# Kernel tuning notes

Measured on AMD Instinct MI355X. Metric: run time of the kernel, lower is better.

Reference implementation:

```python
import jax, jax.numpy as jnp
import numpy as np


def setup_inputs() -> dict:
    key = jax.random.key(0)
    k1, k2 = jax.random.split(key)
    B, S, N, D = 4, 8, 2048, 3
    pred_points = jax.random.normal(k1, (B, S, N, D), dtype=jnp.float32)
    target_points = jax.random.normal(k2, (B, S, N, D), dtype=jnp.float32)
    return {"pred_points": pred_points, "target_points": target_points}


def reference(pred_points, target_points):
    # pred_points, target_points: [B, S, N, 3]
    seq_len = pred_points.shape[1]
    # Pairwise Euclidean distances via the GEMM identity |p-t|^2 = |p|^2 + |t|^2 - 2 p.t
    p2 = jnp.sum(pred_points * pred_points, axis=-1)      # [B,S,N]
    t2 = jnp.sum(target_points * target_points, axis=-1)  # [B,S,M]
    cross = jnp.einsum('bsnd,bsmd->bsnm', pred_points, target_points)  # [B,S,N,M]
    d2 = p2[..., :, None] + t2[..., None, :] - 2.0 * cross
    d = jnp.sqrt(jnp.maximum(d2, 0.0))  # [B,S,N,M]
    # Bidirectional nearest-neighbor min + mean over points
    min_p2t = jnp.min(d, axis=3)  # [B,S,N]
    min_t2p = jnp.min(d, axis=2)  # [B,S,M]
    chamfer = jnp.mean(min_p2t, axis=2) + jnp.mean(min_t2p, axis=2)  # [B,S]
    total_loss = jnp.sum(chamfer, axis=1)  # [B] (sum over timesteps)
    # reduction == 'mean'
    return jnp.mean(total_loss) / seq_len
```

## Files before the change

### kernel.cpp

```cpp
#include <hip/hip_runtime.h>
#include <math.h>

#define N_PTS   2048
#define BLOCK   256
#define NQ      8
#define SLAB    256
#define NSLAB   (N_PTS / SLAB)

__global__ __launch_bounds__(BLOCK) void chamfer_min_kernel(
    const float* __restrict__ pred,
    const float* __restrict__ tgt,
    unsigned int* __restrict__ wsmin)
{
    __shared__ float4 sh[SLAB];

    const int bs   = blockIdx.x;
    const int dir  = blockIdx.y;
    const int slab = blockIdx.z;
    const int tid  = threadIdx.x;

    const float* Abase = (dir ? tgt : pred) + (size_t)bs * N_PTS * 3;
    const float* Bbase = (dir ? pred : tgt) + (size_t)bs * N_PTS * 3;

    {
        const int j = slab * SLAB + tid;
        const float x = Bbase[3 * j + 0];
        const float y = Bbase[3 * j + 1];
        const float z = Bbase[3 * j + 2];
        sh[tid] = make_float4(x, y, z, x * x + y * y + z * z);
    }
    __syncthreads();

    float nx[NQ], ny[NQ], nz[NQ], p2[NQ], best[NQ];
    #pragma unroll
    for (int k = 0; k < NQ; ++k) {
        const int q = tid + BLOCK * k;
        const float px = Abase[3 * q + 0];
        const float py = Abase[3 * q + 1];
        const float pz = Abase[3 * q + 2];
        nx[k] = -2.0f * px;
        ny[k] = -2.0f * py;
        nz[k] = -2.0f * pz;
        p2[k] = px * px + py * py + pz * pz;
        best[k] = 3.4e38f;
    }

    #pragma unroll 2
    for (int j = 0; j < SLAB; j += 2) {
        const float4 t0 = sh[j];
        const float4 t1 = sh[j + 1];
        #pragma unroll
        for (int k = 0; k < NQ; ++k) {
            const float v0 = fmaf(nx[k], t0.x,
                             fmaf(ny[k], t0.y,
                             fmaf(nz[k], t0.z, t0.w)));
            const float v1 = fmaf(nx[k], t1.x,
                             fmaf(ny[k], t1.y,
                             fmaf(nz[k], t1.z, t1.w)));
            best[k] = fminf(fminf(best[k], v0), v1);
        }
    }

    const int base = (dir * 32 + bs) * N_PTS;
    #pragma unroll
    for (int k = 0; k < NQ; ++k) {
        const float d2 = fmaxf(p2[k] + best[k], 0.0f);
        atomicMin(&wsmin[base + tid + BLOCK * k], __float_as_uint(d2));
    }
}

__global__ __launch_bounds__(BLOCK) void chamfer_finalize_kernel(
    const float4* __restrict__ wsmin,
    float* __restrict__ out)
{
    __shared__ float red[BLOCK / 64];
    const int i = blockIdx.x * BLOCK + threadIdx.x;
    const float4 t = wsmin[i];
    float s = sqrtf(t.x) + sqrtf(t.y) + sqrtf(t.z) + sqrtf(t.w);

    for (int off = 32; off > 0; off >>= 1)
        s += __shfl_down(s, off, 64);
    const int tid = threadIdx.x;
    if ((tid & 63) == 0) red[tid >> 6] = s;
    __syncthreads();
    if (tid == 0) {
        const float blk = red[0] + red[1] + red[2] + red[3];
        atomicAdd(out, blk * (1.0f / 65536.0f));
    }
}

extern "C" void kernel_launch(void* const* d_in, const int* in_sizes, int n_in,
                              void* d_out, int out_size, void* d_ws, size_t ws_size,
                              hipStream_t stream) {
    const float* pred = (const float*)d_in[0];
    const float* tgt  = (const float*)d_in[1];
    float* out = (float*)d_out;
    unsigned int* wsmin = (unsigned int*)d_ws;

    hipMemsetAsync(wsmin, 0x7F, (size_t)131072 * sizeof(unsigned int), stream);
    hipMemsetAsync(out, 0, sizeof(float), stream);

    dim3 grid(32, 2, NSLAB);
    chamfer_min_kernel<<<grid, BLOCK, 0, stream>>>(pred, tgt, wsmin);

    chamfer_finalize_kernel<<<131072 / (BLOCK * 4), BLOCK, 0, stream>>>(
        (const float4*)wsmin, out);
}
```

Baseline: 81.90 us.

## Fuse finalize into min kernel via last-block-done counters

Merges the finalize kernel into the min kernel. Per-group atomic counters pick the last slab block, which reduces that group's minima. A global counter then picks the last group, which writes the final mean directly. One memset now initialises the minima, the counters and the partials together (counters start from the 0x7F7F7F7F pattern), replacing the two memsets and the second launch. This removes a kernel launch and a memset in exchange for threadfences, extra atomics and serialized tail work.

```diff
diff --git a/kernel.cpp b/kernel.cpp
--- a/kernel.cpp
+++ b/kernel.cpp
@@ -6,13 +6,23 @@
 #define NQ      8
 #define SLAB    256
 #define NSLAB   (N_PTS / SLAB)
+#define NGRP    64
+#define PBASE   0x7F7F7F7Fu
 
-__global__ __launch_bounds__(BLOCK) void chamfer_min_kernel(
+__global__ __launch_bounds__(BLOCK) void chamfer_fused(
     const float* __restrict__ pred,
     const float* __restrict__ tgt,
-    unsigned int* __restrict__ wsmin)
+    unsigned int* __restrict__ ws,
+    float* __restrict__ out)
 {
     __shared__ float4 sh[SLAB];
+    __shared__ float red[BLOCK / 64];
+    __shared__ int flag;
+
+    unsigned int* wsmin = ws;
+    unsigned int* cnt   = ws + 131072;
+    unsigned int* gdone = ws + 131072 + 64;
+    unsigned int* gpart = ws + 131072 + 65;
 
     const int bs   = blockIdx.x;
     const int dir  = blockIdx.y;
@@ -61,31 +71,48 @@
         }
     }
 
-    const int base = (dir * 32 + bs) * N_PTS;
+    const int g    = dir * 32 + bs;
+    const int base = g * N_PTS;
     #pragma unroll
     for (int k = 0; k < NQ; ++k) {
         const float d2 = fmaxf(p2[k] + best[k], 0.0f);
         atomicMin(&wsmin[base + tid + BLOCK * k], __float_as_uint(d2));
     }
-}
 
-__global__ __launch_bounds__(BLOCK) void chamfer_finalize_kernel(
-    const float4* __restrict__ wsmin,
-    float* __restrict__ out)
-{
-    __shared__ float red[BLOCK / 64];
-    const int i = blockIdx.x * BLOCK + threadIdx.x;
-    const float4 t = wsmin[i];
-    float s = sqrtf(t.x) + sqrtf(t.y) + sqrtf(t.z) + sqrtf(t.w);
+    __threadfence();
+    __syncthreads();
+    if (tid == 0)
+        flag = (atomicAdd(&cnt[g], 1u) == PBASE + (NSLAB - 1)) ? 1 : 0;
+    __syncthreads();
 
-    for (int off = 32; off > 0; off >>= 1)
-        s += __shfl_down(s, off, 64);
-    const int tid = threadIdx.x;
-    if ((tid & 63) == 0) red[tid >> 6] = s;
-    __syncthreads();
-    if (tid == 0) {
-        const float blk = red[0] + red[1] + red[2] + red[3];
-        atomicAdd(out, blk * (1.0f / 65536.0f));
+    if (flag) {
+        float s = 0.0f;
+        #pragma unroll
+        for (int u = 0; u < NQ; ++u) {
+            const unsigned int b =
+                atomicMin(&wsmin[base + tid + BLOCK * u], 0xFFFFFFFFu);
+            s += sqrtf(__uint_as_float(b));
+        }
+        for (int off = 32; off > 0; off >>= 1)
+            s += __shfl_down(s, off, 64);
+        if ((tid & 63) == 0) red[tid >> 6] = s;
+        __syncthreads();
+
+        if (tid == 0) {
+            const float blk = red[0] + red[1] + red[2] + red[3];
+            atomicExch(&gpart[g], __float_as_uint(blk));
+            __threadfence();
+            flag = (atomicAdd(gdone, 1u) == PBASE + (NGRP - 1)) ? 2 : 1;
+        }
+        __syncthreads();
+
+        if (flag == 2 && tid < 64) {
+            float v = __uint_as_float(atomicMin(&gpart[tid], 0xFFFFFFFFu));
+            for (int off = 32; off > 0; off >>= 1)
+                v += __shfl_down(v, off, 64);
+            if (tid == 0)
+                out[0] = v * (1.0f / 65536.0f);
+        }
     }
 }
 
@@ -95,14 +122,10 @@
     const float* pred = (const float*)d_in[0];
     const float* tgt  = (const float*)d_in[1];
     float* out = (float*)d_out;
-    unsigned int* wsmin = (unsigned int*)d_ws;
+    unsigned int* ws = (unsigned int*)d_ws;
 
-    hipMemsetAsync(wsmin, 0x7F, (size_t)131072 * sizeof(unsigned int), stream);
-    hipMemsetAsync(out, 0, sizeof(float), stream);
+    hipMemsetAsync(ws, 0x7F, (size_t)131201 * sizeof(unsigned int), stream);
 
     dim3 grid(32, 2, NSLAB);
-    chamfer_min_kernel<<<grid, BLOCK, 0, stream>>>(pred, tgt, wsmin);
-
-    chamfer_finalize_kernel<<<131072 / (BLOCK * 4), BLOCK, 0, stream>>>(
-        (const float4*)wsmin, out);
+    chamfer_fused<<<grid, BLOCK, 0, stream>>>(pred, tgt, ws, out);
 }
```

Result: slower. 106.6 us (+30.2%).
